# Kernel tuning notes

Measured on AMD Instinct MI355X. Metric: run time of the kernel, lower is better.

The kernel has to match this reference:

```python
import jax, jax.numpy as jnp
import numpy as np

DELTA = 0.1
NEG_INF = -1e30


def setup_inputs() -> dict:
    key = jax.random.key(0)
    k1, k2, k3, k4 = jax.random.split(key, 4)
    Bs, Bt, D, C = 8192, 8192, 64, 10
    return {
        "src_feas": jax.random.normal(k1, (Bs, D), dtype=jnp.float32),
        "src_labels": jax.random.randint(k2, (Bs,), 0, C, dtype=jnp.int32),
        "tgt_feas": jax.random.normal(k3, (Bt, D), dtype=jnp.float32),
        "tgt_logits": jax.random.normal(k4, (Bt, C), dtype=jnp.float32),
    }


def reference(src_feas, src_labels, tgt_feas, tgt_logits):
    # The original builds the explicit list of positive pairs (i_tgt, j_src)
    # where tgt sample i is 'confident' (top1-top2 logit gap >= delta) and
    # src_labels[j] == argmax(tgt_logits[i]).  The [P, P] score matrix it
    # forms is s[k, l] = src_feas[j_k] . tgt_feas[i_l], which only depends on
    # (j_k, i_l), so sum(diag(log_softmax(s))) collapses to a weighted
    # logsumexp over the [Bs, Bt] cross-domain score matrix. Same math,
    # fully vectorized, order-invariant.
    Bs = src_feas.shape[0]
    C = tgt_logits.shape[1]

    top2 = jax.lax.top_k(tgt_logits, 2)[0]                  # [Bt, 2]
    conf = (top2[:, 0] - top2[:, 1]) >= DELTA               # [Bt]
    cls = jnp.argmax(tgt_logits, axis=1)                    # [Bt]

    # per-class count of source samples
    counts = jnp.zeros((C,), jnp.float32).at[src_labels].add(1.0)  # [C]
    # w[i] = multiplicity of tgt sample i in the pair list
    w = jnp.where(conf, counts[cls], 0.0)                   # [Bt]

    M = src_feas @ tgt_feas.T                               # [Bs, Bt]
    logw = jnp.where(w > 0, jnp.log(jnp.maximum(w, 1.0)), NEG_INF)
    # L[j] = log sum over all pairs l of exp(M[j, i_l])
    L = jax.scipy.special.logsumexp(M + logw[None, :], axis=1)  # [Bs]

    pair_mask = conf[None, :] & (src_labels[:, None] == cls[None, :])  # [Bs, Bt]
    nce_sum = jnp.sum(jnp.where(pair_mask, M - L[:, None], 0.0))
    P = jnp.sum(w)                                          # total pair count
    nce = nce_sum / (-1.0 * Bs * P)
    return nce
```

## Files before the change

### kernel.cpp

```cpp
#include <hip/hip_runtime.h>
#include <hip/hip_bf16.h>

#define BSZ 8192
#define BTZ 8192
#define DD 64
#define NC 10
#define SHIFT2 20.0f
#define LN2 0.69314718055994531f
#define LOG2E 1.44269504088896341f

typedef __attribute__((ext_vector_type(8))) short bf16x8;
typedef __attribute__((ext_vector_type(4))) float f32x4;

#if defined(__has_builtin)
#if __has_builtin(__builtin_amdgcn_exp2f)
#define EXP2(x) __builtin_amdgcn_exp2f(x)
#else
#define EXP2(x) exp2f(x)
#endif
#else
#define EXP2(x) exp2f(x)
#endif

__device__ __forceinline__ unsigned short f2bf_rne(float f) {
    unsigned int u = __float_as_uint(f);
    u += 0x7FFFu + ((u >> 16) & 1u);
    return (unsigned short)(u >> 16);
}

__global__ void kA(const float4* __restrict__ src4, const float4* __restrict__ tgt4,
                   const int* __restrict__ labels,
                   ushort4* __restrict__ srcb, ushort4* __restrict__ tgtb,
                   float* __restrict__ cnt_part) {
    __shared__ float hist[NC];
    int t = threadIdx.x;
    int tid = blockIdx.x * 256 + t;
    float4 s = src4[tid];
    ushort4 os;
    os.x = f2bf_rne(s.x * LOG2E); os.y = f2bf_rne(s.y * LOG2E);
    os.z = f2bf_rne(s.z * LOG2E); os.w = f2bf_rne(s.w * LOG2E);
    srcb[tid] = os;
    float4 v = tgt4[tid];
    ushort4 ot; ot.x = f2bf_rne(v.x); ot.y = f2bf_rne(v.y);
    ot.z = f2bf_rne(v.z); ot.w = f2bf_rne(v.w);
    tgtb[tid] = ot;

    if (blockIdx.x < 32) {
        if (t < NC) hist[t] = 0.0f;
        __syncthreads();
        atomicAdd(&hist[labels[tid]], 1.0f);
        __syncthreads();
        if (t < NC) cnt_part[blockIdx.x * NC + t] = hist[t];
    }
}

__global__ void kB(const float* __restrict__ logits,
                   const float* __restrict__ cnt_part,
                   float* __restrict__ colbias, unsigned char* __restrict__ cls8,
                   float* __restrict__ cc_part, float* __restrict__ S) {
    __shared__ float lcnt[NC];
    __shared__ float hist[NC];
    int t = threadIdx.x;
    int i = blockIdx.x * 256 + t;

    if (t < NC) {
        float c = 0.0f;
        #pragma unroll
        for (int b = 0; b < 32; ++b) c += cnt_part[b * NC + t];
        lcnt[t] = c;
        hist[t] = 0.0f;
    }

    float m1 = -3.0e38f, m2 = -3.0e38f; int cls = 0;
    #pragma unroll
    for (int c = 0; c < NC; ++c) {
        float v = logits[i * NC + c];
        if (v > m1) { m2 = m1; m1 = v; cls = c; }
        else if (v > m2) { m2 = v; }
    }
    bool conf = (m1 - m2) >= 0.1f;
    __syncthreads();
    float cnt = lcnt[cls];
    bool live = conf && (cnt > 0.0f);
    colbias[i] = live ? (log2f(cnt) - SHIFT2) : -1.0e30f;
    cls8[i] = live ? (unsigned char)cls : (unsigned char)255;
    S[i] = 0.0f;
    if (conf) atomicAdd(&hist[cls], 1.0f);
    __syncthreads();
    if (t < NC) cc_part[blockIdx.x * NC + t] = hist[t];
}

__global__ __launch_bounds__(256) void kC(const unsigned short* __restrict__ srcb,
                                          const unsigned short* __restrict__ tgtb,
                                          const float* __restrict__ colbias,
                                          const unsigned char* __restrict__ cls8,
                                          const int* __restrict__ labels,
                                          float* __restrict__ S,
                                          float* __restrict__ term1_part) {
    __shared__ float lds[4][64];
    __shared__ float t1red[4];
    int t = threadIdx.x;
    int w = t >> 6;
    int lane = t & 63;
    int l15 = lane & 15;
    int quad = lane >> 4;
    int colchunk = blockIdx.x & 15;
    int rowg = blockIdx.x >> 4;
    int row_base = rowg * 64;

    bf16x8 a[4][2];
    int rl[4][4];
    #pragma unroll
    for (int mb = 0; mb < 4; ++mb) {
        const bf16x8* p = (const bf16x8*)(srcb + (size_t)(row_base + mb * 16 + l15) * DD + quad * 8);
        a[mb][0] = p[0];
        a[mb][1] = p[4];
        #pragma unroll
        for (int r = 0; r < 4; ++r)
            rl[mb][r] = labels[row_base + mb * 16 + quad * 4 + r];
    }

    float rs[4][4];
    #pragma unroll
    for (int mb = 0; mb < 4; ++mb)
        #pragma unroll
        for (int r = 0; r < 4; ++r) rs[mb][r] = 0.0f;
    float t1p = 0.0f;

    int col0 = colchunk * 512 + w * 128;
    #pragma unroll 2
    for (int ct = 0; ct < 8; ++ct) {
        int cb = col0 + ct * 16;
        const bf16x8* q = (const bf16x8*)(tgtb + (size_t)(cb + l15) * DD + quad * 8);
        bf16x8 b0 = q[0];
        bf16x8 b1 = q[4];
        float cb2 = colbias[cb + l15];
        int ccls = (int)cls8[cb + l15];
        #pragma unroll
        for (int mb = 0; mb < 4; ++mb) {
            f32x4 acc = {cb2, cb2, cb2, cb2};
            acc = __builtin_amdgcn_mfma_f32_16x16x32_bf16(a[mb][0], b0, acc, 0, 0, 0);
            acc = __builtin_amdgcn_mfma_f32_16x16x32_bf16(a[mb][1], b1, acc, 0, 0, 0);
            #pragma unroll
            for (int r = 0; r < 4; ++r) {
                float e = acc[r];
                rs[mb][r] += EXP2(e);
                t1p += (ccls == rl[mb][r]) ? (e - cb2) : 0.0f;
            }
        }
    }

    #pragma unroll
    for (int mb = 0; mb < 4; ++mb) {
        #pragma unroll
        for (int r = 0; r < 4; ++r) {
            float v = rs[mb][r];
            v += __shfl_xor(v, 1);
            v += __shfl_xor(v, 2);
            v += __shfl_xor(v, 4);
            v += __shfl_xor(v, 8);
            if (l15 == 0) lds[w][mb * 16 + quad * 4 + r] = v;
        }
    }
    float tv = t1p;
    #pragma unroll
    for (int m = 1; m < 64; m <<= 1) tv += __shfl_xor(tv, m);
    if (lane == 0) t1red[w] = tv;
    __syncthreads();
    if (t < 64)
        atomicAdd(&S[row_base + t], lds[0][t] + lds[1][t] + lds[2][t] + lds[3][t]);
    if (t == 128)
        term1_part[blockIdx.x] = t1red[0] + t1red[1] + t1red[2] + t1red[3];
}

__global__ void kD(const float* __restrict__ S, const int* __restrict__ labels,
                   const float* __restrict__ cnt_part, const float* __restrict__ cc_part,
                   const float* __restrict__ term1_part,
                   float* __restrict__ out) {
    __shared__ float counts[NC], cc[NC];
    int t = threadIdx.x;
    if (t < NC) {
        float c0 = 0.0f, c1 = 0.0f;
        #pragma unroll
        for (int b = 0; b < 32; ++b) { c0 += cnt_part[b * NC + t]; c1 += cc_part[b * NC + t]; }
        counts[t] = c0; cc[t] = c1;
    }
    __syncthreads();

    float termL = 0.0f, term1 = 0.0f, P = 0.0f;
    for (int j = t; j < BSZ; j += 256) {
        float L = (log2f(S[j]) + SHIFT2) * LN2;
        termL += cc[labels[j]] * L;
    }
    for (int o = t; o < 2048; o += 256) term1 += term1_part[o];
    if (t < NC) P = counts[t] * cc[t];

    __shared__ float redL[4], red1[4], redP[4];
    int w = t >> 6, lane = t & 63;
    float v1 = termL, v2 = term1, v3 = P;
    #pragma unroll
    for (int m = 1; m < 64; m <<= 1) {
        v1 += __shfl_xor(v1, m);
        v2 += __shfl_xor(v2, m);
        v3 += __shfl_xor(v3, m);
    }
    if (lane == 0) { redL[w] = v1; red1[w] = v2; redP[w] = v3; }
    __syncthreads();
    if (t == 0) {
        float tl = redL[0] + redL[1] + redL[2] + redL[3];
        float t1 = (red1[0] + red1[1] + red1[2] + red1[3]) * LN2;
        float p  = redP[0] + redP[1] + redP[2] + redP[3];
        out[0] = (t1 - tl) / (-(float)BSZ * p);
    }
}

extern "C" void kernel_launch(void* const* d_in, const int* in_sizes, int n_in,
                              void* d_out, int out_size, void* d_ws, size_t ws_size,
                              hipStream_t stream) {
    const float* src    = (const float*)d_in[0];
    const int*   labels = (const int*)d_in[1];
    const float* tgt    = (const float*)d_in[2];
    const float* logits = (const float*)d_in[3];

    char* ws = (char*)d_ws;
    float* S          = (float*)(ws + 0);
    float* cnt_part   = (float*)(ws + 32768);
    float* cc_part    = (float*)(ws + 34048);
    float* term1_part = (float*)(ws + 35328);
    float* colbias    = (float*)(ws + 65536);
    unsigned char* cls8 = (unsigned char*)(ws + 98304);
    unsigned short* srcb = (unsigned short*)(ws + 131072);
    unsigned short* tgtb = (unsigned short*)(ws + 131072 + 1048576);

    kA<<<512, 256, 0, stream>>>((const float4*)src, (const float4*)tgt, labels,
                                (ushort4*)srcb, (ushort4*)tgtb, cnt_part);
    kB<<<32, 256, 0, stream>>>(logits, cnt_part, colbias, cls8, cc_part, S);
    kC<<<2048, 256, 0, stream>>>(srcb, tgtb, colbias, cls8, labels, S, term1_part);
    kD<<<1, 256, 0, stream>>>(S, labels, cnt_part, cc_part, term1_part, (float*)d_out);
}
```

Baseline: 109.9 us.

## Compact live target columns, factor positive-pair term via class sums, fuse kernels

```diff
diff --git a/kernel.cpp b/kernel.cpp
--- a/kernel.cpp
+++ b/kernel.cpp
@@ -28,48 +28,59 @@
     return (unsigned short)(u >> 16);
 }
 
-__global__ void kA(const float4* __restrict__ src4, const float4* __restrict__ tgt4,
-                   const int* __restrict__ labels,
-                   ushort4* __restrict__ srcb, ushort4* __restrict__ tgtb,
-                   float* __restrict__ cnt_part) {
-    __shared__ float hist[NC];
+__global__ __launch_bounds__(256) void kAB(
+    const float4* __restrict__ src4, const float4* __restrict__ tgt4,
+    const int* __restrict__ labels, const float* __restrict__ logits,
+    ushort4* __restrict__ srcb, ushort4* __restrict__ tgtb,
+    float* __restrict__ S, float* __restrict__ counts,
+    float* __restrict__ cc_part, unsigned char* __restrict__ cls8,
+    float* __restrict__ cbias_c, int* __restrict__ cidx,
+    int* __restrict__ gcursor)
+{
     int t = threadIdx.x;
-    int tid = blockIdx.x * 256 + t;
-    float4 s = src4[tid];
-    ushort4 os;
-    os.x = f2bf_rne(s.x * LOG2E); os.y = f2bf_rne(s.y * LOG2E);
-    os.z = f2bf_rne(s.z * LOG2E); os.w = f2bf_rne(s.w * LOG2E);
-    srcb[tid] = os;
-    float4 v = tgt4[tid];
-    ushort4 ot; ot.x = f2bf_rne(v.x); ot.y = f2bf_rne(v.y);
-    ot.z = f2bf_rne(v.z); ot.w = f2bf_rne(v.w);
-    tgtb[tid] = ot;
-
-    if (blockIdx.x < 32) {
-        if (t < NC) hist[t] = 0.0f;
-        __syncthreads();
-        atomicAdd(&hist[labels[tid]], 1.0f);
-        __syncthreads();
-        if (t < NC) cnt_part[blockIdx.x * NC + t] = hist[t];
-    }
-}
-
-__global__ void kB(const float* __restrict__ logits,
-                   const float* __restrict__ cnt_part,
-                   float* __restrict__ colbias, unsigned char* __restrict__ cls8,
-                   float* __restrict__ cc_part, float* __restrict__ S) {
+    if (blockIdx.x < 512) {
+        int tid = blockIdx.x * 256 + t;
+        float4 s = src4[tid];
+        ushort4 os;
+        os.x = f2bf_rne(s.x * LOG2E); os.y = f2bf_rne(s.y * LOG2E);
+        os.z = f2bf_rne(s.z * LOG2E); os.w = f2bf_rne(s.w * LOG2E);
+        srcb[tid] = os;
+        float4 v = tgt4[tid];
+        ushort4 ot; ot.x = f2bf_rne(v.x); ot.y = f2bf_rne(v.y);
+        ot.z = f2bf_rne(v.z); ot.w = f2bf_rne(v.w);
+        tgtb[tid] = ot;
+        return;
+    }
     __shared__ float lcnt[NC];
     __shared__ float hist[NC];
-    int t = threadIdx.x;
-    int i = blockIdx.x * 256 + t;
-
-    if (t < NC) {
-        float c = 0.0f;
-        #pragma unroll
-        for (int b = 0; b < 32; ++b) c += cnt_part[b * NC + t];
-        lcnt[t] = c;
-        hist[t] = 0.0f;
-    }
+    __shared__ float hred[4][NC];
+    __shared__ int lpos;
+    __shared__ int lbase;
+    int b = blockIdx.x - 512;
+    int i = b * 256 + t;
+    int w = t >> 6, lane = t & 63;
+
+    float c10[NC];
+    #pragma unroll
+    for (int c = 0; c < NC; ++c) c10[c] = 0.0f;
+    for (int k = 0; k < 32; ++k) {
+        int lab = labels[t + 256 * k];
+        #pragma unroll
+        for (int c = 0; c < NC; ++c) c10[c] += (lab == c) ? 1.0f : 0.0f;
+    }
+    #pragma unroll
+    for (int c = 0; c < NC; ++c) {
+        float v = c10[c];
+        #pragma unroll
+        for (int m = 1; m < 64; m <<= 1) v += __shfl_xor(v, m);
+        if (lane == 0) hred[w][c] = v;
+    }
+    if (t == 0) lpos = 0;
+    if (t < NC) hist[t] = 0.0f;
+    __syncthreads();
+    if (t < NC) lcnt[t] = hred[0][t] + hred[1][t] + hred[2][t] + hred[3][t];
+    __syncthreads();
+    if (b == 0 && t < NC) counts[t] = lcnt[t];
 
     float m1 = -3.0e38f, m2 = -3.0e38f; int cls = 0;
     #pragma unroll
@@ -79,27 +90,56 @@
         else if (v > m2) { m2 = v; }
     }
     bool conf = (m1 - m2) >= 0.1f;
-    __syncthreads();
     float cnt = lcnt[cls];
     bool live = conf && (cnt > 0.0f);
-    colbias[i] = live ? (log2f(cnt) - SHIFT2) : -1.0e30f;
     cls8[i] = live ? (unsigned char)cls : (unsigned char)255;
     S[i] = 0.0f;
     if (conf) atomicAdd(&hist[cls], 1.0f);
-    __syncthreads();
-    if (t < NC) cc_part[blockIdx.x * NC + t] = hist[t];
-}
-
-__global__ __launch_bounds__(256) void kC(const unsigned short* __restrict__ srcb,
-                                          const unsigned short* __restrict__ tgtb,
-                                          const float* __restrict__ colbias,
-                                          const unsigned char* __restrict__ cls8,
-                                          const int* __restrict__ labels,
-                                          float* __restrict__ S,
-                                          float* __restrict__ term1_part) {
+    int myp = 0;
+    if (live) myp = atomicAdd(&lpos, 1);
+    __syncthreads();
+    if (t < NC) cc_part[b * NC + t] = hist[t];
+    if (t == 0) lbase = atomicAdd(gcursor, lpos);
+    __syncthreads();
+    if (live) {
+        cidx[lbase + myp] = i;
+        cbias_c[lbase + myp] = log2f(cnt) - SHIFT2;
+    }
+}
+
+__global__ __launch_bounds__(256) void kC(
+    const unsigned short* __restrict__ srcb, const unsigned short* __restrict__ tgtb,
+    const float* __restrict__ cbias_c, const int* __restrict__ cidx,
+    const int* __restrict__ gcursor, float* __restrict__ S,
+    const float* __restrict__ srcf, const float* __restrict__ tgtf,
+    const int* __restrict__ labels, const unsigned char* __restrict__ cls8,
+    float* __restrict__ SC, float* __restrict__ T)
+{
+    int t = threadIdx.x;
+    if (blockIdx.x >= 2048) {
+        int bb = blockIdx.x - 2048;
+        bool isT = bb >= 32;
+        int rb = (bb & 31) * 256;
+        const float* F = isT ? tgtf : srcf;
+        int w = t >> 6, lane = t & 63;
+        float acc[NC];
+        #pragma unroll
+        for (int c = 0; c < NC; ++c) acc[c] = 0.0f;
+        int row0 = rb + w * 64;
+        for (int r = 0; r < 64; ++r) {
+            int row = row0 + r;
+            int lab = isT ? (int)cls8[row] : labels[row];
+            float f = F[row * DD + lane];
+            #pragma unroll
+            for (int c = 0; c < NC; ++c) acc[c] += (lab == c) ? f : 0.0f;
+        }
+        float* OUT = isT ? T : SC;
+        #pragma unroll
+        for (int c = 0; c < NC; ++c) atomicAdd(&OUT[c * DD + lane], acc[c]);
+        return;
+    }
+
     __shared__ float lds[4][64];
-    __shared__ float t1red[4];
-    int t = threadIdx.x;
     int w = t >> 6;
     int lane = t & 63;
     int l15 = lane & 15;
@@ -107,17 +147,15 @@
     int colchunk = blockIdx.x & 15;
     int rowg = blockIdx.x >> 4;
     int row_base = rowg * 64;
+    int Pn = *gcursor;
+    if (colchunk * 512 >= Pn) return;
 
     bf16x8 a[4][2];
-    int rl[4][4];
     #pragma unroll
     for (int mb = 0; mb < 4; ++mb) {
         const bf16x8* p = (const bf16x8*)(srcb + (size_t)(row_base + mb * 16 + l15) * DD + quad * 8);
         a[mb][0] = p[0];
         a[mb][1] = p[4];
-        #pragma unroll
-        for (int r = 0; r < 4; ++r)
-            rl[mb][r] = labels[row_base + mb * 16 + quad * 4 + r];
     }
 
     float rs[4][4];
@@ -125,28 +163,26 @@
     for (int mb = 0; mb < 4; ++mb)
         #pragma unroll
         for (int r = 0; r < 4; ++r) rs[mb][r] = 0.0f;
-    float t1p = 0.0f;
 
     int col0 = colchunk * 512 + w * 128;
     #pragma unroll 2
     for (int ct = 0; ct < 8; ++ct) {
         int cb = col0 + ct * 16;
-        const bf16x8* q = (const bf16x8*)(tgtb + (size_t)(cb + l15) * DD + quad * 8);
+        int cc = cb + l15;
+        bool ok = cc < Pn;
+        int col = ok ? cidx[cc] : 0;
+        float cb2 = ok ? cbias_c[cc] : -1.0e30f;
+        const bf16x8* q = (const bf16x8*)(tgtb + (size_t)col * DD + quad * 8);
         bf16x8 b0 = q[0];
         bf16x8 b1 = q[4];
-        float cb2 = colbias[cb + l15];
-        int ccls = (int)cls8[cb + l15];
         #pragma unroll
         for (int mb = 0; mb < 4; ++mb) {
             f32x4 acc = {cb2, cb2, cb2, cb2};
             acc = __builtin_amdgcn_mfma_f32_16x16x32_bf16(a[mb][0], b0, acc, 0, 0, 0);
             acc = __builtin_amdgcn_mfma_f32_16x16x32_bf16(a[mb][1], b1, acc, 0, 0, 0);
             #pragma unroll
-            for (int r = 0; r < 4; ++r) {
-                float e = acc[r];
-                rs[mb][r] += EXP2(e);
-                t1p += (ccls == rl[mb][r]) ? (e - cb2) : 0.0f;
-            }
+            for (int r = 0; r < 4; ++r)
+                rs[mb][r] += EXP2(acc[r]);
         }
     }
 
@@ -162,55 +198,62 @@
             if (l15 == 0) lds[w][mb * 16 + quad * 4 + r] = v;
         }
     }
-    float tv = t1p;
-    #pragma unroll
-    for (int m = 1; m < 64; m <<= 1) tv += __shfl_xor(tv, m);
-    if (lane == 0) t1red[w] = tv;
     __syncthreads();
     if (t < 64)
         atomicAdd(&S[row_base + t], lds[0][t] + lds[1][t] + lds[2][t] + lds[3][t]);
-    if (t == 128)
-        term1_part[blockIdx.x] = t1red[0] + t1red[1] + t1red[2] + t1red[3];
-}
-
-__global__ void kD(const float* __restrict__ S, const int* __restrict__ labels,
-                   const float* __restrict__ cnt_part, const float* __restrict__ cc_part,
-                   const float* __restrict__ term1_part,
-                   float* __restrict__ out) {
-    __shared__ float counts[NC], cc[NC];
+}
+
+__global__ __launch_bounds__(256) void kD(
+    const float* __restrict__ S, const int* __restrict__ labels,
+    const float* __restrict__ counts, const float* __restrict__ cc_part,
+    const float* __restrict__ SC, const float* __restrict__ T,
+    float* __restrict__ gACC, int* __restrict__ gcnt,
+    float* __restrict__ out)
+{
+    __shared__ float cc[NC];
+    __shared__ float redL[4], red1[4], redP[4];
+    __shared__ int isLast;
     int t = threadIdx.x;
+    int w = t >> 6, lane = t & 63;
     if (t < NC) {
-        float c0 = 0.0f, c1 = 0.0f;
-        #pragma unroll
-        for (int b = 0; b < 32; ++b) { c0 += cnt_part[b * NC + t]; c1 += cc_part[b * NC + t]; }
-        counts[t] = c0; cc[t] = c1;
-    }
-    __syncthreads();
-
-    float termL = 0.0f, term1 = 0.0f, P = 0.0f;
-    for (int j = t; j < BSZ; j += 256) {
-        float L = (log2f(S[j]) + SHIFT2) * LN2;
-        termL += cc[labels[j]] * L;
-    }
-    for (int o = t; o < 2048; o += 256) term1 += term1_part[o];
-    if (t < NC) P = counts[t] * cc[t];
-
-    __shared__ float redL[4], red1[4], redP[4];
-    int w = t >> 6, lane = t & 63;
-    float v1 = termL, v2 = term1, v3 = P;
+        float s = 0.0f;
+        #pragma unroll
+        for (int k = 0; k < 32; ++k) s += cc_part[k * NC + t];
+        cc[t] = s;
+    }
+    __syncthreads();
+    int j = blockIdx.x * 256 + t;
+    float L = (log2f(S[j]) + SHIFT2) * LN2;
+    float tl = cc[labels[j]] * L;
+    #pragma unroll
+    for (int m = 1; m < 64; m <<= 1) tl += __shfl_xor(tl, m);
+    if (lane == 0) redL[w] = tl;
+    __syncthreads();
+    if (t == 0) {
+        float v = redL[0] + redL[1] + redL[2] + redL[3];
+        atomicAdd(&gACC[0], v);
+        __threadfence();
+        int old = atomicAdd(gcnt, 1);
+        isLast = (old == 31) ? 1 : 0;
+    }
+    __syncthreads();
+    if (!isLast) return;
+
+    float t1 = 0.0f;
+    for (int o = t; o < NC * DD; o += 256) t1 += SC[o] * T[o];
+    float Pp = (t < NC) ? counts[t] * cc[t] : 0.0f;
     #pragma unroll
     for (int m = 1; m < 64; m <<= 1) {
-        v1 += __shfl_xor(v1, m);
-        v2 += __shfl_xor(v2, m);
-        v3 += __shfl_xor(v3, m);
-    }
-    if (lane == 0) { redL[w] = v1; red1[w] = v2; redP[w] = v3; }
+        t1 += __shfl_xor(t1, m);
+        Pp += __shfl_xor(Pp, m);
+    }
+    if (lane == 0) { red1[w] = t1; redP[w] = Pp; }
     __syncthreads();
     if (t == 0) {
-        float tl = redL[0] + redL[1] + redL[2] + redL[3];
-        float t1 = (red1[0] + red1[1] + red1[2] + red1[3]) * LN2;
-        float p  = redP[0] + redP[1] + redP[2] + redP[3];
-        out[0] = (t1 - tl) / (-(float)BSZ * p);
+        float term1 = red1[0] + red1[1] + red1[2] + red1[3];
+        float P = redP[0] + redP[1] + redP[2] + redP[3];
+        float termL = atomicAdd(&gACC[0], 0.0f);
+        out[0] = (term1 - termL) / (-(float)BSZ * P);
     }
 }
 
@@ -223,18 +266,26 @@
     const float* logits = (const float*)d_in[3];
 
     char* ws = (char*)d_ws;
-    float* S          = (float*)(ws + 0);
-    float* cnt_part   = (float*)(ws + 32768);
-    float* cc_part    = (float*)(ws + 34048);
-    float* term1_part = (float*)(ws + 35328);
-    float* colbias    = (float*)(ws + 65536);
-    unsigned char* cls8 = (unsigned char*)(ws + 98304);
-    unsigned short* srcb = (unsigned short*)(ws + 131072);
-    unsigned short* tgtb = (unsigned short*)(ws + 131072 + 1048576);
-
-    kA<<<512, 256, 0, stream>>>((const float4*)src, (const float4*)tgt, labels,
-                                (ushort4*)srcb, (ushort4*)tgtb, cnt_part);
-    kB<<<32, 256, 0, stream>>>(logits, cnt_part, colbias, cls8, cc_part, S);
-    kC<<<2048, 256, 0, stream>>>(srcb, tgtb, colbias, cls8, labels, S, term1_part);
-    kD<<<1, 256, 0, stream>>>(S, labels, cnt_part, cc_part, term1_part, (float*)d_out);
-}
+    float* S        = (float*)(ws + 0);
+    int*   gcursor  = (int*)(ws + 32768);
+    int*   gcnt     = (int*)(ws + 32772);
+    float* gACC     = (float*)(ws + 32776);
+    float* counts   = (float*)(ws + 32784);
+    float* cc_part  = (float*)(ws + 32832);
+    float* SC       = (float*)(ws + 34112);
+    float* T        = (float*)(ws + 36672);
+    float* cbias_c  = (float*)(ws + 40960);
+    int*   cidx     = (int*)(ws + 73728);
+    unsigned char* cls8 = (unsigned char*)(ws + 106496);
+    unsigned short* srcb = (unsigned short*)(ws + 114688);
+    unsigned short* tgtb = (unsigned short*)(ws + 114688 + 1048576);
+
+    hipMemsetAsync(ws + 32768, 0, 8192, stream);
+    kAB<<<544, 256, 0, stream>>>((const float4*)src, (const float4*)tgt, labels,
+                                 logits, (ushort4*)srcb, (ushort4*)tgtb,
+                                 S, counts, cc_part, cls8, cbias_c, cidx, gcursor);
+    kC<<<2112, 256, 0, stream>>>(srcb, tgtb, cbias_c, cidx, gcursor, S,
+                                 src, tgt, labels, cls8, SC, T);
+    kD<<<32, 256, 0, stream>>>(S, labels, counts, cc_part, SC, T,
+                               gACC, gcnt, (float*)d_out);
+}
```

Result: slower. 122.1 us (+11.1%).
